# Kernel tuning notes

Measured on AMD Instinct MI355X. Metric: run time of the kernel, lower is better.

## Reference

```python
import jax, jax.numpy as jnp
import numpy as np

C_IN, H, W = 8, 32, 32
C_OUT, K, S, P = 32, 4, 2, 1
HO = (H + 2 * P - K) // S + 1  # 16
WO = (W + 2 * P - K) // S + 1  # 16
IN_FEAT = C_IN * H * W          # 8192
OUT_FEAT = C_OUT * HO * WO      # 8192


def conv2d(x, w, b=None):
    # x: [N, C_in, H, W], w: [C_out, C_in, K, K]
    y = jax.lax.conv_general_dilated(
        x, w, window_strides=(S, S), padding=[(P, P), (P, P)],
        dimension_numbers=("NCHW", "OIHW", "NCHW"))
    if b is not None:
        y = y + b[None, :, None, None]
    return y


def toeplitz_matrix(weight):
    # Equivalent to torch.autograd.functional.jacobian of flatten(conv(x)):
    # conv is linear, so apply it to the identity basis (batched conv).
    eye = jnp.eye(IN_FEAT, dtype=weight.dtype).reshape(IN_FEAT, C_IN, H, W)
    cols = conv2d(eye, weight).reshape(IN_FEAT, OUT_FEAT)  # column j = conv(e_j)
    return cols.T  # [OUT_FEAT, IN_FEAT]


def setup_inputs() -> dict:
    key = jax.random.key(0)
    k1, k2, k3, k4 = jax.random.split(key, 4)
    center = jax.random.normal(k1, (C_IN, H, W), jnp.float32)
    eps = 0.01 * jax.random.uniform(k2, (C_IN, H, W), jnp.float32)
    bounds = jnp.stack([center - eps, center + eps], 0)  # [2, C_in, H, W]
    weight = 0.1 * jax.random.normal(k3, (C_OUT, C_IN, K, K), jnp.float32)
    bias = 0.1 * jax.random.normal(k4, (C_OUT,), jnp.float32)
    assignment = jnp.zeros((C_OUT, HO, WO), jnp.int32)  # unused by forward
    return {"bounds": bounds, "weight": weight, "bias": bias,
            "assignment": assignment}


def reference(bounds, weight, bias, assignment):
    W_plus = jnp.maximum(weight, 0.0)
    W_minus = jnp.minimum(weight, 0.0)
    half_b = bias / 2.0
    l = bounds[0][None]  # [1, C_in, H, W]
    u = bounds[1][None]
    # upper = conv_plus(u) + conv_minus(l); each conv carries bias/2
    upper = conv2d(u, W_plus, half_b) + conv2d(l, W_minus, half_b)
    lower = conv2d(l, W_plus, half_b) + conv2d(u, W_minus, half_b)
    out_bounds = jnp.concatenate([lower, upper], 0)  # [2, C_out, HO, WO]

    # back-substitution (terminal branch: predecessor is the input layer)
    W_mat = toeplitz_matrix(weight)                 # [OUT_FEAT, IN_FEAT]
    bias_backsub = jnp.repeat(bias, HO * WO)        # repeat_interleave
    Mp = jnp.maximum(W_mat, 0.0)
    Mm = jnp.minimum(W_mat, 0.0)
    lf = bounds[0].reshape(-1)
    uf = bounds[1].reshape(-1)
    new_l = (Mp @ lf + Mm @ uf + bias_backsub).reshape(C_OUT, HO, WO)
    new_u = (Mp @ uf + Mm @ lf + bias_backsub).reshape(C_OUT, HO, WO)
    # tighten: keep the better of forward-propagated and back-substituted
    out_bounds = out_bounds.at[0].set(jnp.where(new_l > out_bounds[0], new_l, out_bounds[0]))
    out_bounds = out_bounds.at[1].set(jnp.where(new_u < out_bounds[1], new_u, out_bounds[1]))
    return out_bounds, W_mat, bias_backsub
```

## Files before the change

### kernel.cpp

```cpp
#include <hip/hip_runtime.h>

#define C_IN   8
#define HH     32
#define WW     32
#define C_OUT  32
#define KK     4
#define SS     2
#define PP     1
#define HO     16
#define WO     16
#define IN_FEAT  8192
#define OUT_FEAT 8192

typedef float f32x4 __attribute__((ext_vector_type(4)));

__global__ __launch_bounds__(256) void fused_row_kernel(const float* __restrict__ bounds,
                                                        const float* __restrict__ weight,
                                                        const float* __restrict__ bias,
                                                        float* __restrict__ wmat,
                                                        float* __restrict__ out_bounds,
                                                        float* __restrict__ bias_bs) {
    const int gid  = blockIdx.x * 256 + threadIdx.x;
    const int row  = gid >> 6;
    const int lane = threadIdx.x & 63;

    const int c_out = row >> 8;
    const int ho    = (row >> 4) & 15;
    const int wo    = row & 15;
    const int hs    = ho * SS - PP;
    const int ws    = wo * SS - PP;

    const int  lh   = lane >> 3;
    const int  w0   = (lane & 7) * 4;
    const int  kwb  = w0 - ws;
    const bool whit = (kwb >= -3) & (kwb <= 3);

    unsigned hbmask = 0;
    {
        const int loh = hs > 0 ? hs : 0;
        const int hih = (hs + 3) < 31 ? (hs + 3) : 31;
#pragma unroll
        for (int hb = 0; hb < 4; ++hb)
            if (hb * 8 <= hih && loh <= hb * 8 + 7) hbmask |= 1u << hb;
    }
    hbmask = __builtin_amdgcn_readfirstlane(hbmask);

    const f32x4 zero4 = (f32x4){0.f, 0.f, 0.f, 0.f};
    f32x4* __restrict__ rp = reinterpret_cast<f32x4*>(wmat + (size_t)row * IN_FEAT) + lane;
    const float* __restrict__ wco = weight + c_out * (C_IN * KK * KK);

    for (int ci = 0; ci < C_IN; ++ci) {
#pragma unroll
        for (int hb = 0; hb < 4; ++hb, rp += 64) {
            if (hbmask & (1u << hb)) {
                f32x4 v = zero4;
                const int kh = hb * 8 + lh - hs;
                if (((unsigned)kh < (unsigned)KK) & whit) {
                    const float* wb = wco + ci * (KK * KK) + kh * KK;
#pragma unroll
                    for (int j = 0; j < 4; ++j) {
                        const int kw = kwb + j;
                        if ((unsigned)kw < (unsigned)KK) v[j] = wb[kw];
                    }
                }
                __builtin_nontemporal_store(v, rp);
            } else {
                __builtin_nontemporal_store(zero4, rp);
            }
        }
    }

    const float* lptr = bounds;
    const float* uptr = bounds + IN_FEAT;
    float lo = 0.f, up = 0.f;
#pragma unroll
    for (int s = 0; s < 2; ++s) {
        const int t  = lane + 64 * s;
        const int ci = t >> 4;
        const int kh = (t >> 2) & 3;
        const int kw = t & 3;
        const int h  = hs + kh;
        const int w  = ws + kw;
        if ((unsigned)h < (unsigned)HH && (unsigned)w < (unsigned)WW) {
            const float wv  = wco[ci * (KK * KK) + kh * KK + kw];
            const int   col = ci * (HH * WW) + h * WW + w;
            const float lv = lptr[col];
            const float uv = uptr[col];
            const float wp = fmaxf(wv, 0.f);
            const float wm = fminf(wv, 0.f);
            lo = fmaf(wp, lv, fmaf(wm, uv, lo));
            up = fmaf(wp, uv, fmaf(wm, lv, up));
        }
    }
#pragma unroll
    for (int off = 32; off; off >>= 1) {
        lo += __shfl_down(lo, off, 64);
        up += __shfl_down(up, off, 64);
    }
    if (lane == 0) {
        const float b = bias[c_out];
        out_bounds[row]            = lo + b;
        out_bounds[OUT_FEAT + row] = up + b;
        bias_bs[row] = b;
    }
}

extern "C" void kernel_launch(void* const* d_in, const int* in_sizes, int n_in,
                              void* d_out, int out_size, void* d_ws, size_t ws_size,
                              hipStream_t stream) {
    const float* bounds = (const float*)d_in[0];
    const float* weight = (const float*)d_in[1];
    const float* bias   = (const float*)d_in[2];

    float* out     = (float*)d_out;
    float* wmat    = out + 2 * OUT_FEAT;
    float* bias_bs = out + 2 * OUT_FEAT + (size_t)OUT_FEAT * IN_FEAT;

    fused_row_kernel<<<2048, 256, 0, stream>>>(bounds, weight, bias, wmat, out, bias_bs);
}
```

Measured before the change: 260.8 us.

## Split Toeplitz write into bulk zero-fill kernel plus sparse tap scatter

Replaces the fused per-row kernel, which computed every 16-byte chunk of each W_mat row, with two kernels. The first is a plain grid-stride zero fill of the whole 256 MB matrix. The second scatters only the nonzero weight taps and computes the bounds. This removes per-chunk index arithmetic and branching from the bandwidth-bound store stream. In exchange it adds a second launch, drops the nontemporal store hint, and makes the scatter kernel issue scattered single-float writes that depend on ordering after the fill.

```diff
diff --git a/kernel.cpp b/kernel.cpp
--- a/kernel.cpp
+++ b/kernel.cpp
@@ -11,15 +11,24 @@
 #define WO     16
 #define IN_FEAT  8192
 #define OUT_FEAT 8192
+#define WMAT_QUADS (OUT_FEAT * IN_FEAT / 4)
 
 typedef float f32x4 __attribute__((ext_vector_type(4)));
 
-__global__ __launch_bounds__(256) void fused_row_kernel(const float* __restrict__ bounds,
-                                                        const float* __restrict__ weight,
-                                                        const float* __restrict__ bias,
-                                                        float* __restrict__ wmat,
-                                                        float* __restrict__ out_bounds,
-                                                        float* __restrict__ bias_bs) {
+
+__global__ __launch_bounds__(256) void zero_wmat(f32x4* __restrict__ p) {
+    const f32x4 z = (f32x4){0.f, 0.f, 0.f, 0.f};
+    const int stride = gridDim.x * 256;
+    for (int i = blockIdx.x * 256 + threadIdx.x; i < WMAT_QUADS; i += stride)
+        p[i] = z;
+}
+
+__global__ __launch_bounds__(256) void scatter_taps(const float* __restrict__ bounds,
+                                                    const float* __restrict__ weight,
+                                                    const float* __restrict__ bias,
+                                                    float* __restrict__ wmat,
+                                                    float* __restrict__ out_bounds,
+                                                    float* __restrict__ bias_bs) {
     const int gid  = blockIdx.x * 256 + threadIdx.x;
     const int row  = gid >> 6;
     const int lane = threadIdx.x & 63;
@@ -30,48 +39,11 @@
     const int hs    = ho * SS - PP;
     const int ws    = wo * SS - PP;
 
-    const int  lh   = lane >> 3;
-    const int  w0   = (lane & 7) * 4;
-    const int  kwb  = w0 - ws;
-    const bool whit = (kwb >= -3) & (kwb <= 3);
+    const float* __restrict__ wco  = weight + c_out * (C_IN * KK * KK);
+    const float* __restrict__ lptr = bounds;
+    const float* __restrict__ uptr = bounds + IN_FEAT;
+    float* __restrict__ wrow = wmat + (size_t)row * IN_FEAT;
 
-    unsigned hbmask = 0;
-    {
-        const int loh = hs > 0 ? hs : 0;
-        const int hih = (hs + 3) < 31 ? (hs + 3) : 31;
-#pragma unroll
-        for (int hb = 0; hb < 4; ++hb)
-            if (hb * 8 <= hih && loh <= hb * 8 + 7) hbmask |= 1u << hb;
-    }
-    hbmask = __builtin_amdgcn_readfirstlane(hbmask);
-
-    const f32x4 zero4 = (f32x4){0.f, 0.f, 0.f, 0.f};
-    f32x4* __restrict__ rp = reinterpret_cast<f32x4*>(wmat + (size_t)row * IN_FEAT) + lane;
-    const float* __restrict__ wco = weight + c_out * (C_IN * KK * KK);
-
-    for (int ci = 0; ci < C_IN; ++ci) {
-#pragma unroll
-        for (int hb = 0; hb < 4; ++hb, rp += 64) {
-            if (hbmask & (1u << hb)) {
-                f32x4 v = zero4;
-                const int kh = hb * 8 + lh - hs;
-                if (((unsigned)kh < (unsigned)KK) & whit) {
-                    const float* wb = wco + ci * (KK * KK) + kh * KK;
-#pragma unroll
-                    for (int j = 0; j < 4; ++j) {
-                        const int kw = kwb + j;
-                        if ((unsigned)kw < (unsigned)KK) v[j] = wb[kw];
-                    }
-                }
-                __builtin_nontemporal_store(v, rp);
-            } else {
-                __builtin_nontemporal_store(zero4, rp);
-            }
-        }
-    }
-
-    const float* lptr = bounds;
-    const float* uptr = bounds + IN_FEAT;
     float lo = 0.f, up = 0.f;
 #pragma unroll
     for (int s = 0; s < 2; ++s) {
@@ -84,6 +56,7 @@
         if ((unsigned)h < (unsigned)HH && (unsigned)w < (unsigned)WW) {
             const float wv  = wco[ci * (KK * KK) + kh * KK + kw];
             const int   col = ci * (HH * WW) + h * WW + w;
+            wrow[col] = wv;
             const float lv = lptr[col];
             const float uv = uptr[col];
             const float wp = fmaxf(wv, 0.f);
@@ -116,5 +89,6 @@
     float* wmat    = out + 2 * OUT_FEAT;
     float* bias_bs = out + 2 * OUT_FEAT + (size_t)OUT_FEAT * IN_FEAT;
 
-    fused_row_kernel<<<2048, 256, 0, stream>>>(bounds, weight, bias, wmat, out, bias_bs);
+    zero_wmat<<<2048, 256, 0, stream>>>(reinterpret_cast<f32x4*>(wmat));
+    scatter_taps<<<2048, 256, 0, stream>>>(bounds, weight, bias, wmat, out, bias_bs);
 }
```

Result: slower. 273.5 us (+4.8%).
